# Optimization experiments

Hardware: AMD Instinct MI355X
Metric: run time of the kernel (lower is better)

## Reference

```python
import jax, jax.numpy as jnp
import numpy as np

B, T, H = 4, 4096, 1024


def setup_inputs() -> dict:
    key = jax.random.key(0)
    k1, k2 = jax.random.split(key)
    h = jax.random.normal(k1, (B, T, H), dtype=jnp.float32)
    # nn.Linear weight, scaled for stable magnitudes
    W = jax.random.normal(k2, (H, H), dtype=jnp.float32) / np.sqrt(H).astype(np.float32)
    return {"h": h, "W": W, "T_hist": 256}


def reference(h, W, T_hist):
    Bb, Tt, Hh = h.shape
    # K = Linear(h) = h @ W.T ; Q = V = h
    K = jnp.einsum('bth,oh->bto', h, W)
    scores = jnp.einsum('bqh,bkh->bqk', h, K) / jnp.sqrt(jnp.asarray(Hh, h.dtype))
    # banded mask: causal (j <= i) AND limited history (j >= i - (T_hist-1))
    i = jnp.arange(Tt)[:, None]
    j = jnp.arange(Tt)[None, :]
    valid = (j <= i) & (j >= i - (T_hist - 1))
    scores = jnp.where(valid[None, :, :], scores, -jnp.inf)
    attn = jax.nn.softmax(scores, axis=-1)
    attn = jnp.nan_to_num(attn, nan=0.0)  # matches torch nan_to_num(0.0)
    context = jnp.einsum('bqk,bkh->bqh', attn, h)
    return context
```

## Files before the change

kernel.cpp:

```cpp
#include <hip/hip_runtime.h>
#include <hip/hip_bf16.h>

#define B_ 4
#define T_ 4096
#define H_ 1024
#define WP2 320

typedef short  s16x8 __attribute__((ext_vector_type(8)));
typedef float  f32x4 __attribute__((ext_vector_type(4)));
typedef unsigned short u16;

static __device__ __forceinline__ u16 bf16rn(float f) {
  unsigned int u = __float_as_uint(f);
  u += 0x7fffu + ((u >> 16) & 1u);
  return (u16)(u >> 16);
}

static __device__ __forceinline__ void gl2lds16(const u16* g, u16* l) {
  __builtin_amdgcn_global_load_lds(
      (__attribute__((address_space(1))) void*)(g),
      (__attribute__((address_space(3))) void*)(l), 16, 0, 0);
}

__global__ __launch_bounds__(256) void k_convT(const float* __restrict__ h,
                                               u16* __restrict__ hb,
                                               u16* __restrict__ hbT) {
  __shared__ u16 tile[64][72];
  const int b  = blockIdx.z;
  const int t0 = blockIdx.y * 64;
  const int c0 = blockIdx.x * 64;
  const int t  = threadIdx.x;
  {
    const int r  = t >> 2;
    const int cq = (t & 3) << 4;
    const size_t g = (size_t)(b * T_ + t0 + r) * H_ + c0 + cq;
    const f32x4* src = (const f32x4*)(h + g);
    u16 o[16];
#pragma unroll
    for (int v = 0; v < 4; ++v) {
      f32x4 x = src[v];
#pragma unroll
      for (int j = 0; j < 4; ++j) o[v * 4 + j] = bf16rn(x[j]);
    }
    s16x8 w0, w1;
#pragma unroll
    for (int j = 0; j < 8; ++j) { w0[j] = (short)o[j]; w1[j] = (short)o[8 + j]; }
    *(s16x8*)(hb + g)     = w0;
    *(s16x8*)(hb + g + 8) = w1;
    *(s16x8*)&tile[r][cq]     = w0;
    *(s16x8*)&tile[r][cq + 8] = w1;
  }
  __syncthreads();
  {
    const int c  = t >> 2;
    const int ch = t & 3;
#pragma unroll
    for (int p = 0; p < 2; ++p) {
      const int k0 = (ch + p * 4) * 8;
      s16x8 w;
#pragma unroll
      for (int j = 0; j < 8; ++j) w[j] = (short)tile[k0 + j][c];
      *(s16x8*)(hbT + (size_t)(b * H_ + c0 + c) * T_ + t0 + k0) = w;
    }
  }
}

__global__ __launch_bounds__(256) void k_convW(const float* __restrict__ src,
                                               u16* __restrict__ dst) {
  const int i = (blockIdx.x * 256 + threadIdx.x) * 8;
  f32x4 a = *(const f32x4*)(src + i);
  f32x4 b = *(const f32x4*)(src + i + 4);
  s16x8 w;
#pragma unroll
  for (int j = 0; j < 4; ++j) {
    w[j]     = (short)bf16rn(a[j]);
    w[4 + j] = (short)bf16rn(b[j]);
  }
  *(s16x8*)(dst + i) = w;
}

__global__ __launch_bounds__(256) void k_gemmK(const u16* __restrict__ hb,
                                               const u16* __restrict__ Wb,
                                               u16* __restrict__ Kb) {
  __shared__ __align__(16) u16 As[512 * 8];
  __shared__ __align__(16) u16 Bs[512 * 8];
  const int t = threadIdx.x;
  const int row0 = blockIdx.y * 128;
  const int col0 = blockIdx.x * 128;
  const int lane = t & 63, wv = t >> 6;
  const int wr = wv >> 1, wc = wv & 1;
  const int l15 = lane & 15, quad = lane >> 4;

  const int c0 = t, c1 = t + 256;
  const size_t gA0 = (size_t)(row0 + (c0 >> 2)) * H_ + (c0 & 3) * 8;
  const size_t gA1 = (size_t)(row0 + (c1 >> 2)) * H_ + (c1 & 3) * 8;
  const size_t gB0 = (size_t)(col0 + (c0 >> 2)) * H_ + (c0 & 3) * 8;
  const size_t gB1 = (size_t)(col0 + (c1 >> 2)) * H_ + (c1 & 3) * 8;

  f32x4 acc[4][4];
#pragma unroll
  for (int m = 0; m < 4; ++m)
#pragma unroll
    for (int n = 0; n < 4; ++n) acc[m][n] = (f32x4)0.0f;

  for (int k0 = 0; k0 < H_; k0 += 32) {
    __syncthreads();
    gl2lds16(hb + gA0 + k0, &As[c0 * 8]);
    gl2lds16(hb + gA1 + k0, &As[c1 * 8]);
    gl2lds16(Wb + gB0 + k0, &Bs[c0 * 8]);
    gl2lds16(Wb + gB1 + k0, &Bs[c1 * 8]);
    __syncthreads();
    s16x8 aF[4], bF[4];
#pragma unroll
    for (int mt = 0; mt < 4; ++mt)
      aF[mt] = *(const s16x8*)&As[((wr * 64 + mt * 16 + l15) * 4 + quad) * 8];
#pragma unroll
    for (int nt = 0; nt < 4; ++nt)
      bF[nt] = *(const s16x8*)&Bs[((wc * 64 + nt * 16 + l15) * 4 + quad) * 8];
#pragma unroll
    for (int mt = 0; mt < 4; ++mt)
#pragma unroll
      for (int nt = 0; nt < 4; ++nt)
        acc[mt][nt] = __builtin_amdgcn_mfma_f32_16x16x32_bf16(aF[mt], bF[nt],
                                                              acc[mt][nt], 0, 0, 0);
  }
#pragma unroll
  for (int mt = 0; mt < 4; ++mt)
#pragma unroll
    for (int nt = 0; nt < 4; ++nt)
#pragma unroll
      for (int r = 0; r < 4; ++r) {
        const int row = row0 + wr * 64 + mt * 16 + quad * 4 + r;
        const int col = col0 + wc * 64 + nt * 16 + l15;
        Kb[(size_t)row * H_ + col] = bf16rn(acc[mt][nt][r]);
      }
}

__global__ __launch_bounds__(512) void k_scores(const u16* __restrict__ hb,
                                                const u16* __restrict__ Kb,
                                                u16* __restrict__ P) {
  __shared__ __align__(16) u16 Ks[2304 * 8];
  __shared__ float Sred[2][4][16];
  const int t = threadIdx.x;
  const int wv = t >> 6, lane = t & 63;
  const int l15 = lane & 15, quad = lane >> 4;
  const int blk = blockIdx.x;
  const int b = blk >> 7;
  const int q0 = (blk & 127) * 32;
  const int qt = wv & 1;
  const int sub = wv >> 1;
  const int qt0 = q0 + qt * 16;
  const int ktbase = (sub == 0) ? 0 : (1 + sub * 4);
  const int nkt = (sub == 0) ? 5 : 4;

  const int npass = (t < 256) ? 5 : 4;
  size_t goff[5];
#pragma unroll
  for (int p = 0; p < 5; ++p) {
    int c = p * 512 + t;
    if (c > 2303) c = 2303;
    const int m = c >> 7, kk = (c >> 6) & 1, lr = (c >> 2) & 15, qd = c & 3;
    int tok = q0 - 256 + m * 16 + lr;
    if (tok < 0) tok = 0;
    goff[p] = (size_t)(b * T_ + tok) * H_ + kk * 32 + qd * 8;
  }
  const u16* qbase = hb + (size_t)(b * T_ + qt0 + l15) * H_ + quad * 8;

  f32x4 acc[5];
#pragma unroll
  for (int i = 0; i < 5; ++i) acc[i] = (f32x4)0.0f;

  for (int hh = 0; hh < H_; hh += 64) {
    __syncthreads();
#pragma unroll
    for (int p = 0; p < 5; ++p)
      if (p < npass) gl2lds16(Kb + goff[p] + hh, &Ks[(p * 512 + t) * 8]);
    __syncthreads();
#pragma unroll
    for (int kk = 0; kk < 2; ++kk) {
      const s16x8 aQ = *(const s16x8*)(qbase + hh + kk * 32);
#pragma unroll
      for (int i = 0; i < 5; ++i) {
        if (i < nkt) {
          const int m = qt + ktbase + i;
          const s16x8 bK =
              *(const s16x8*)&Ks[((m * 2 + kk) * 64 + l15 * 4 + quad) * 8];
          acc[i] = __builtin_amdgcn_mfma_f32_16x16x32_bf16(aQ, bK, acc[i], 0, 0, 0);
        }
      }
    }
  }

  const float scale = 0.03125f;
#pragma unroll
  for (int r = 0; r < 4; ++r) {
    const int q = qt0 + quad * 4 + r;
    float sum = 0.0f;
#pragma unroll
    for (int i = 0; i < 5; ++i) {
      if (i < nkt) {
        const int k = qt0 - 256 + (ktbase + i) * 16 + l15;
        const bool valid = (k >= 0) && (k <= q) && (k >= q - 255);
        const float p = valid ? __expf(acc[i][r] * scale) : 0.0f;
        acc[i][r] = p;
        sum += p;
      }
    }
    sum += __shfl_xor(sum, 1);
    sum += __shfl_xor(sum, 2);
    sum += __shfl_xor(sum, 4);
    sum += __shfl_xor(sum, 8);
    if (l15 == 0) Sred[qt][sub][quad * 4 + r] = sum;
  }
  __syncthreads();
  const int toff = ((q0 & 32) >> 4) + qt;
#pragma unroll
  for (int r = 0; r < 4; ++r) {
    const int q = qt0 + quad * 4 + r;
    const int row = quad * 4 + r;
    const float inv = 1.0f / (Sred[qt][0][row] + Sred[qt][1][row] +
                              Sred[qt][2][row] + Sred[qt][3][row]);
    u16* prow = P + (size_t)(b * T_ + q) * WP2;
#pragma unroll
    for (int i = 0; i < 5; ++i)
      if (i < nkt) prow[(toff + ktbase + i) * 16 + l15] = bf16rn(acc[i][r] * inv);
    if (sub == 0) {
#pragma unroll
      for (int z = 0; z < 3; ++z) {
        const int slot = (toff + 17 + z) % 20;
        prow[slot * 16 + l15] = 0;
      }
    }
  }
}

__global__ __launch_bounds__(512) void k_ctx(const u16* __restrict__ P,
                                             const u16* __restrict__ hbT,
                                             float* __restrict__ out) {
  __shared__ __align__(16) u16 Vs[2560 * 8];
  const int t = threadIdx.x;
  const int wv = t >> 6, lane = t & 63;
  const int l15 = lane & 15, quad = lane >> 4;
  const int fhalf = blockIdx.x;
  const int blk = blockIdx.y;
  const int b = blk >> 6;
  const int q0 = (blk & 63) * 64;
  const int qtile = wv & 3, fh = wv >> 2;
  const int qt0 = q0 + qtile * 16;

  const u16* prow = P + (size_t)(b * T_ + qt0 + l15) * WP2 + quad * 8;
  s16x8 aP[10];
#pragma unroll
  for (int c = 0; c < 10; ++c) aP[c] = *(const s16x8*)(prow + c * 32);

  const int tok0 = q0 - 256;
  size_t goff[5];
#pragma unroll
  for (int p = 0; p < 5; ++p) {
    const int c = p * 512 + t;
    const int cg = c >> 8, ft = (c >> 6) & 3, lr = (c >> 2) & 15, qd = c & 3;
    const int fr = ft * 16 + lr;
    int tok = tok0 + (cg * 4 + qd) * 8;
    if (tok < 0) tok = 0;
    goff[p] = (size_t)(b * H_ + fr) * T_ + tok;
  }

  for (int f8 = 0; f8 < 8; ++f8) {
    const int f0 = (fhalf * 8 + f8) * 64;
    __syncthreads();
#pragma unroll
    for (int p = 0; p < 5; ++p)
      gl2lds16(hbT + goff[p] + (size_t)f0 * T_, &Vs[(p * 512 + t) * 8]);
    __syncthreads();
    f32x4 acc0 = (f32x4)0.0f, acc1 = (f32x4)0.0f;
#pragma unroll
    for (int c = 0; c < 10; ++c) {
      const s16x8 bv0 =
          *(const s16x8*)&Vs[(c * 256 + (fh * 2 + 0) * 64 + l15 * 4 + quad) * 8];
      acc0 = __builtin_amdgcn_mfma_f32_16x16x32_bf16(aP[c], bv0, acc0, 0, 0, 0);
      const s16x8 bv1 =
          *(const s16x8*)&Vs[(c * 256 + (fh * 2 + 1) * 64 + l15 * 4 + quad) * 8];
      acc1 = __builtin_amdgcn_mfma_f32_16x16x32_bf16(aP[c], bv1, acc1, 0, 0, 0);
    }
#pragma unroll
    for (int r = 0; r < 4; ++r) {
      const size_t orow = (size_t)(b * T_ + qt0 + quad * 4 + r) * H_ + f0;
      out[orow + (fh * 2 + 0) * 16 + l15] = acc0[r];
      out[orow + (fh * 2 + 1) * 16 + l15] = acc1[r];
    }
  }
}

extern "C" void kernel_launch(void* const* d_in, const int* in_sizes, int n_in,
                              void* d_out, int out_size, void* d_ws, size_t ws_size,
                              hipStream_t stream) {
  const float* h  = (const float*)d_in[0];
  const float* Wf = (const float*)d_in[1];

  char* ws = (char*)d_ws;
  u16* hb  = (u16*)(ws);
  u16* hbT = (u16*)(ws + (size_t)33554432);
  u16* Kb  = (u16*)(ws + (size_t)67108864);
  u16* Wb  = (u16*)(ws + (size_t)100663296);
  u16* P   = (u16*)(ws + (size_t)102760448);
  float* out = (float*)d_out;

  k_convT <<<dim3(H_ / 64, T_ / 64, B_), 256, 0, stream>>>(h, hb, hbT);
  k_convW <<<dim3(512), 256, 0, stream>>>(Wf, Wb);
  k_gemmK <<<dim3(H_ / 128, (B_ * T_) / 128), 256, 0, stream>>>(hb, Wb, Kb);
  k_scores<<<dim3((B_ * T_) / 32), 512, 0, stream>>>(hb, Kb, P);
  k_ctx   <<<dim3(2, (B_ * T_) / 64), 512, 0, stream>>>(P, hbT, out);
}
```

Before: 265.4 us.

## Drop LDS staging in scores/context kernels and swizzle block order for XCD locality

Removes the shared-memory staging and barriers in k_scores and k_ctx, so each wave reads K and V fragments straight from global memory (relying on L1/L2 for reuse). It also remaps block indices in the GEMM, scores and context kernels so that blocks landing on the same XCD (id&7) cover contiguous tiles, aiming for better L2 locality. The context kernel grid is flattened to 1D to support the swizzle. The risk is redundant global loads across waves that previously shared one LDS tile, and uncoalesced 16-byte strided reads.

```diff
diff --git a/kernel.cpp b/kernel.cpp
--- a/kernel.cpp
+++ b/kernel.cpp
@@ -85,8 +85,10 @@
   __shared__ __align__(16) u16 As[512 * 8];
   __shared__ __align__(16) u16 Bs[512 * 8];
   const int t = threadIdx.x;
-  const int row0 = blockIdx.y * 128;
-  const int col0 = blockIdx.x * 128;
+  const int id  = blockIdx.y * gridDim.x + blockIdx.x;
+  const int swz = (id & 7) * 128 + (id >> 3);
+  const int row0 = (swz >> 3) * 128;
+  const int col0 = (swz & 7) * 128;
   const int lane = t & 63, wv = t >> 6;
   const int wr = wv >> 1, wc = wv & 1;
   const int l15 = lane & 15, quad = lane >> 4;
@@ -139,52 +141,43 @@
 __global__ __launch_bounds__(512) void k_scores(const u16* __restrict__ hb,
                                                 const u16* __restrict__ Kb,
                                                 u16* __restrict__ P) {
-  __shared__ __align__(16) u16 Ks[2304 * 8];
   __shared__ float Sred[2][4][16];
   const int t = threadIdx.x;
   const int wv = t >> 6, lane = t & 63;
   const int l15 = lane & 15, quad = lane >> 4;
-  const int blk = blockIdx.x;
-  const int b = blk >> 7;
-  const int q0 = (blk & 127) * 32;
+  const int id  = blockIdx.x;
+  const int swz = (id & 7) * 64 + (id >> 3);
+  const int b  = swz >> 7;
+  const int q0 = (swz & 127) * 32;
   const int qt = wv & 1;
   const int sub = wv >> 1;
   const int qt0 = q0 + qt * 16;
   const int ktbase = (sub == 0) ? 0 : (1 + sub * 4);
   const int nkt = (sub == 0) ? 5 : 4;
 
-  const int npass = (t < 256) ? 5 : 4;
-  size_t goff[5];
-#pragma unroll
-  for (int p = 0; p < 5; ++p) {
-    int c = p * 512 + t;
-    if (c > 2303) c = 2303;
-    const int m = c >> 7, kk = (c >> 6) & 1, lr = (c >> 2) & 15, qd = c & 3;
-    int tok = q0 - 256 + m * 16 + lr;
+  const u16* qbase = hb + (size_t)(b * T_ + qt0 + l15) * H_ + quad * 8;
+
+  const u16* kbas[5];
+#pragma unroll
+  for (int i = 0; i < 5; ++i) {
+    int tok = q0 - 256 + (qt + ktbase + i) * 16 + l15;
     if (tok < 0) tok = 0;
-    goff[p] = (size_t)(b * T_ + tok) * H_ + kk * 32 + qd * 8;
-  }
-  const u16* qbase = hb + (size_t)(b * T_ + qt0 + l15) * H_ + quad * 8;
+    kbas[i] = Kb + (size_t)(b * T_ + tok) * H_ + quad * 8;
+  }
 
   f32x4 acc[5];
 #pragma unroll
   for (int i = 0; i < 5; ++i) acc[i] = (f32x4)0.0f;
 
+#pragma unroll
   for (int hh = 0; hh < H_; hh += 64) {
-    __syncthreads();
-#pragma unroll
-    for (int p = 0; p < 5; ++p)
-      if (p < npass) gl2lds16(Kb + goff[p] + hh, &Ks[(p * 512 + t) * 8]);
-    __syncthreads();
 #pragma unroll
     for (int kk = 0; kk < 2; ++kk) {
       const s16x8 aQ = *(const s16x8*)(qbase + hh + kk * 32);
 #pragma unroll
       for (int i = 0; i < 5; ++i) {
         if (i < nkt) {
-          const int m = qt + ktbase + i;
-          const s16x8 bK =
-              *(const s16x8*)&Ks[((m * 2 + kk) * 64 + l15 * 4 + quad) * 8];
+          const s16x8 bK = *(const s16x8*)(kbas[i] + hh + kk * 32);
           acc[i] = __builtin_amdgcn_mfma_f32_16x16x32_bf16(aQ, bK, acc[i], 0, 0, 0);
         }
       }
@@ -237,13 +230,14 @@
 __global__ __launch_bounds__(512) void k_ctx(const u16* __restrict__ P,
                                              const u16* __restrict__ hbT,
                                              float* __restrict__ out) {
-  __shared__ __align__(16) u16 Vs[2560 * 8];
   const int t = threadIdx.x;
   const int wv = t >> 6, lane = t & 63;
   const int l15 = lane & 15, quad = lane >> 4;
-  const int fhalf = blockIdx.x;
-  const int blk = blockIdx.y;
-  const int b = blk >> 6;
+  const int id  = blockIdx.x;
+  const int swz = (id & 7) * 64 + (id >> 3);
+  const int fhalf = swz & 1;
+  const int blk   = swz >> 1;
+  const int b  = blk >> 6;
   const int q0 = (blk & 63) * 64;
   const int qtile = wv & 3, fh = wv >> 2;
   const int qt0 = q0 + qtile * 16;
@@ -254,33 +248,34 @@
   for (int c = 0; c < 10; ++c) aP[c] = *(const s16x8*)(prow + c * 32);
 
   const int tok0 = q0 - 256;
-  size_t goff[5];
-#pragma unroll
-  for (int p = 0; p < 5; ++p) {
-    const int c = p * 512 + t;
-    const int cg = c >> 8, ft = (c >> 6) & 3, lr = (c >> 2) & 15, qd = c & 3;
-    const int fr = ft * 16 + lr;
-    int tok = tok0 + (cg * 4 + qd) * 8;
-    if (tok < 0) tok = 0;
-    goff[p] = (size_t)(b * H_ + fr) * T_ + tok;
-  }
 
   for (int f8 = 0; f8 < 8; ++f8) {
     const int f0 = (fhalf * 8 + f8) * 64;
-    __syncthreads();
-#pragma unroll
-    for (int p = 0; p < 5; ++p)
-      gl2lds16(hbT + goff[p] + (size_t)f0 * T_, &Vs[(p * 512 + t) * 8]);
-    __syncthreads();
+    const int g0 = f0 + (fh * 2 + 0) * 16 + l15;
+    const int g1 = f0 + (fh * 2 + 1) * 16 + l15;
+    const u16* vb0 = hbT + (size_t)(b * H_ + g0) * T_;
+    const u16* vb1 = hbT + (size_t)(b * H_ + g1) * T_;
     f32x4 acc0 = (f32x4)0.0f, acc1 = (f32x4)0.0f;
-#pragma unroll
-    for (int c = 0; c < 10; ++c) {
-      const s16x8 bv0 =
-          *(const s16x8*)&Vs[(c * 256 + (fh * 2 + 0) * 64 + l15 * 4 + quad) * 8];
-      acc0 = __builtin_amdgcn_mfma_f32_16x16x32_bf16(aP[c], bv0, acc0, 0, 0, 0);
-      const s16x8 bv1 =
-          *(const s16x8*)&Vs[(c * 256 + (fh * 2 + 1) * 64 + l15 * 4 + quad) * 8];
-      acc1 = __builtin_amdgcn_mfma_f32_16x16x32_bf16(aP[c], bv1, acc1, 0, 0, 0);
+    if (tok0 >= 0) {
+      const u16* v0 = vb0 + tok0 + quad * 8;
+      const u16* v1 = vb1 + tok0 + quad * 8;
+#pragma unroll
+      for (int c = 0; c < 10; ++c) {
+        const s16x8 bv0 = *(const s16x8*)(v0 + c * 32);
+        acc0 = __builtin_amdgcn_mfma_f32_16x16x32_bf16(aP[c], bv0, acc0, 0, 0, 0);
+        const s16x8 bv1 = *(const s16x8*)(v1 + c * 32);
+        acc1 = __builtin_amdgcn_mfma_f32_16x16x32_bf16(aP[c], bv1, acc1, 0, 0, 0);
+      }
+    } else {
+#pragma unroll
+      for (int c = 0; c < 10; ++c) {
+        int tok = tok0 + c * 32 + quad * 8;
+        if (tok < 0) tok = 0;
+        const s16x8 bv0 = *(const s16x8*)(vb0 + tok);
+        acc0 = __builtin_amdgcn_mfma_f32_16x16x32_bf16(aP[c], bv0, acc0, 0, 0, 0);
+        const s16x8 bv1 = *(const s16x8*)(vb1 + tok);
+        acc1 = __builtin_amdgcn_mfma_f32_16x16x32_bf16(aP[c], bv1, acc1, 0, 0, 0);
+      }
     }
 #pragma unroll
     for (int r = 0; r < 4; ++r) {
@@ -309,5 +304,5 @@
   k_convW <<<dim3(512), 256, 0, stream>>>(Wf, Wb);
   k_gemmK <<<dim3(H_ / 128, (B_ * T_) / 128), 256, 0, stream>>>(hb, Wb, Kb);
   k_scores<<<dim3((B_ * T_) / 32), 512, 0, stream>>>(hb, Kb, P);
-  k_ctx   <<<dim3(2, (B_ * T_) / 64), 512, 0, stream>>>(P, hbT, out);
-}
+  k_ctx   <<<dim3(2 * (B_ * T_) / 64), 512, 0, stream>>>(P, hbT, out);
+}
```

After: 329.4 us. +24.1%, slower.
